# Kernel optimization log

Hardware: AMD Instinct MI355X
Metric: run time of the kernel (lower is better)

Reference implementation:

```python
import jax, jax.numpy as jnp
import numpy as np

EPS = 1e-5
SLOPE = 0.01  # InPlaceABNSync default: leaky_relu(0.01)
SIZES = (1, 2, 3, 6)


def adaptive_avg_pool(x, oh, ow):
    # Matches torch floor/ceil window rule via integral image (single fused op).
    N, C, H, W = x.shape
    S = jnp.pad(x, ((0, 0), (0, 0), (1, 0), (1, 0))).cumsum(2).cumsum(3)
    hs = np.floor(np.arange(oh) * H / oh).astype(np.int32)
    he = np.ceil((np.arange(oh) + 1) * H / oh).astype(np.int32)
    ws = np.floor(np.arange(ow) * W / ow).astype(np.int32)
    we = np.ceil((np.arange(ow) + 1) * W / ow).astype(np.int32)
    sums = (S[:, :, he][:, :, :, we] - S[:, :, hs][:, :, :, we]
            - S[:, :, he][:, :, :, ws] + S[:, :, hs][:, :, :, ws])
    area = ((he - hs)[:, None] * (we - ws)[None, :]).astype(x.dtype)
    return sums / area


def bn_lrelu(x, gamma, beta):
    # BatchNorm (training-mode batch stats, biased var) + leaky_relu, per InPlaceABNSync.
    mean = x.mean((0, 2, 3), keepdims=True)
    var = x.var((0, 2, 3), keepdims=True)
    y = (x - mean) * jax.lax.rsqrt(var + EPS) * gamma[None, :, None, None] + beta[None, :, None, None]
    return jnp.where(y >= 0, y, SLOPE * y)


def upsample_bilinear_ac(x, H, W):
    # align_corners=True bilinear, separable along H then W
    N, C, h, w = x.shape
    yc = jnp.arange(H, dtype=x.dtype) * ((h - 1) / (H - 1) if H > 1 else 0.0)
    xc = jnp.arange(W, dtype=x.dtype) * ((w - 1) / (W - 1) if W > 1 else 0.0)
    y0 = jnp.floor(yc).astype(jnp.int32); y1 = jnp.minimum(y0 + 1, h - 1)
    x0 = jnp.floor(xc).astype(jnp.int32); x1 = jnp.minimum(x0 + 1, w - 1)
    wy = (yc - y0.astype(x.dtype))[None, None, :, None]
    wx = (xc - x0.astype(x.dtype))[None, None, None, :]
    xr = x[:, :, y0, :] * (1 - wy) + x[:, :, y1, :] * wy
    return xr[:, :, :, x0] * (1 - wx) + xr[:, :, :, x1] * wx


def conv1x1(x, w):  # w: [O, I]
    return jnp.einsum('nihw,oi->nohw', x, w)


def conv3x3(x, w):  # w: [O, I, 3, 3]
    return jax.lax.conv_general_dilated(x, w, (1, 1), ((1, 1), (1, 1)),
                                        dimension_numbers=('NCHW', 'OIHW', 'NCHW'))


def setup_inputs() -> dict:
    key = jax.random.key(0)
    ks = jax.random.split(key, 20)
    F_in, F_out = 2048, 512
    inp = {'feats': jax.random.normal(ks[0], (2, F_in, 64, 64), jnp.float32)}
    for s in range(4):
        inp[f'w{s}'] = jax.random.normal(ks[1 + s], (F_out, F_in), jnp.float32) * (F_in ** -0.5)
        inp[f'g{s}'] = jnp.ones((F_out,), jnp.float32)
        inp[f'b{s}'] = jnp.zeros((F_out,), jnp.float32)
    inp['wb'] = jax.random.normal(ks[10], (F_out, F_in + 4 * F_out, 3, 3), jnp.float32) * ((9 * (F_in + 4 * F_out)) ** -0.5)
    inp['gb'] = jnp.ones((F_out,), jnp.float32)
    inp['bb'] = jnp.zeros((F_out,), jnp.float32)
    return inp


def reference(feats, w0, g0, b0, w1, g1, b1, w2, g2, b2, w3, g3, b3, wb, gb, bb):
    H, W = feats.shape[2], feats.shape[3]
    ws = [w0, w1, w2, w3]; gs = [g0, g1, g2, g3]; bs = [b0, b1, b2, b3]
    priors = []
    for s, sz in enumerate(SIZES):
        p = adaptive_avg_pool(feats, sz, sz)
        p = bn_lrelu(conv1x1(p, ws[s]), gs[s], bs[s])
        priors.append(upsample_bilinear_ac(p, H, W))
    priors.append(feats)
    cat = jnp.concatenate(priors, axis=1)
    return bn_lrelu(conv3x3(cat, wb), gb, bb)
```

## Files before the change

### kernel.cpp

```cpp
#include <hip/hip_runtime.h>
#include <stdint.h>


typedef short short8 __attribute__((ext_vector_type(8)));
typedef float f32x4 __attribute__((ext_vector_type(4)));
typedef unsigned short us4 __attribute__((ext_vector_type(4)));

#define PADW   66
#define PLANE  (PADW*PADW)
#define PLANE_ELEMS ((size_t)PLANE*64)

#define POOLED_OFF  0u
#define YS_OFF      819200u
#define STATS_OFF   1024000u
#define CAT_OFF     1048576u
#define CAT_BYTES   71368704u
#define PACKED_OFF  (CAT_OFF + CAT_BYTES)
#define PACKED_BYTES 37748736u
#define CBUF_OFF    (PACKED_OFF + PACKED_BYTES)
#define CBUF_BYTES  16777216u

__device__ __forceinline__ unsigned short f2bf(float x) {
  unsigned int u = __float_as_uint(x);
  unsigned int r = (u + 0x7fffu + ((u >> 16) & 1u)) >> 16;
  return (unsigned short)r;
}

__device__ __forceinline__ void load_lds16(const void* g, uint32_t lds_off) {
  __builtin_amdgcn_global_load_lds(
      (__attribute__((address_space(1))) void*)(uintptr_t)g,
      (__attribute__((address_space(3))) void*)(uintptr_t)lds_off,
      16, 0, 0);
}

__global__ __launch_bounds__(256) void pool_kernel(const float* __restrict__ feats,
                                                   float* __restrict__ pooled) {
  __shared__ float rowtot[64];
  __shared__ float rowseg2[64][2];
  __shared__ float rowseg3[64][3];
  __shared__ float rowseg6[64][6];
  const int t = threadIdx.x;
  const int b = blockIdx.x;
  const float* plane = feats + (size_t)b * 4096;
  const int h = t >> 2, w0 = (t & 3) << 4;
  const int ws3[3] = {0, 21, 42}, we3[3] = {22, 43, 64};
  const int ws6[6] = {0, 10, 21, 32, 42, 53}, we6[6] = {11, 22, 32, 43, 54, 64};
  float p3[3] = {0.f, 0.f, 0.f};
  float p6[6] = {0.f, 0.f, 0.f, 0.f, 0.f, 0.f};
  float tot = 0.f;
  const float4* row = (const float4*)(plane + h * 64 + w0);
#pragma unroll
  for (int i4 = 0; i4 < 4; ++i4) {
    float4 v = row[i4];
    float vals[4] = {v.x, v.y, v.z, v.w};
#pragma unroll
    for (int j = 0; j < 4; ++j) {
      const int w = w0 + i4 * 4 + j;
      const float x = vals[j];
      tot += x;
#pragma unroll
      for (int q = 0; q < 3; ++q) if (w >= ws3[q] && w < we3[q]) p3[q] += x;
#pragma unroll
      for (int q = 0; q < 6; ++q) if (w >= ws6[q] && w < we6[q]) p6[q] += x;
    }
  }
  float pair = tot + __shfl_down(tot, 1, 4);
  float tot4 = pair + __shfl_down(pair, 2, 4);
#pragma unroll
  for (int q = 0; q < 3; ++q) {
    p3[q] += __shfl_down(p3[q], 1, 4);
    p3[q] += __shfl_down(p3[q], 2, 4);
  }
#pragma unroll
  for (int q = 0; q < 6; ++q) {
    p6[q] += __shfl_down(p6[q], 1, 4);
    p6[q] += __shfl_down(p6[q], 2, 4);
  }
  if ((t & 3) == 0) {
    rowtot[h] = tot4;
    rowseg2[h][0] = pair;
#pragma unroll
    for (int q = 0; q < 3; ++q) rowseg3[h][q] = p3[q];
#pragma unroll
    for (int q = 0; q < 6; ++q) rowseg6[h][q] = p6[q];
  }
  if ((t & 3) == 2) rowseg2[h][1] = pair;
  __syncthreads();
  if (t < 50) {
    float s = 0.f;
    float inv;
    if (t == 0) {
      for (int r = 0; r < 64; ++r) s += rowtot[r];
      inv = 1.0f / 4096.0f;
    } else if (t < 5) {
      const int qh = (t - 1) >> 1, qw = (t - 1) & 1;
      for (int r = qh * 32; r < qh * 32 + 32; ++r) s += rowseg2[r][qw];
      inv = 1.0f / 1024.0f;
    } else if (t < 14) {
      const int p = t - 5, qh = p / 3, qw = p % 3;
      for (int r = ws3[qh]; r < we3[qh]; ++r) s += rowseg3[r][qw];
      inv = 1.0f / ((float)(we3[qh] - ws3[qh]) * (float)(we3[qw] - ws3[qw]));
    } else {
      const int p = t - 14, qh = p / 6, qw = p % 6;
      for (int r = ws6[qh]; r < we6[qh]; ++r) s += rowseg6[r][qw];
      inv = 1.0f / ((float)(we6[qh] - ws6[qh]) * (float)(we6[qw] - ws6[qw]));
    }
    const int n = b >> 11, c = b & 2047;
    pooled[((size_t)(n * 50 + t)) * 2048 + c] = s * inv;
  }
}

__global__ __launch_bounds__(256) void conv1x1_kernel(
    const float* __restrict__ pooled, const float* __restrict__ w0,
    const float* __restrict__ w1, const float* __restrict__ w2,
    const float* __restrict__ w3, float* __restrict__ ys) {
  __shared__ float xs[512];
  const int t = threadIdx.x;
  const int col = blockIdx.x >> 2;
  const int kq = blockIdx.x & 3;
  const int n = col / 50, spos = col % 50;
  for (int i = t; i < 512; i += 256)
    xs[i] = pooled[(size_t)col * 2048 + kq * 512 + i];
  __syncthreads();
  int si, pos;
  if (spos < 1)       { si = 0; pos = spos; }
  else if (spos < 5)  { si = 1; pos = spos - 1; }
  else if (spos < 14) { si = 2; pos = spos - 5; }
  else                { si = 3; pos = spos - 14; }
  const float* Wt = (si == 0) ? w0 : (si == 1) ? w1 : (si == 2) ? w2 : w3;
  const int ssarr[4] = {1, 4, 9, 36};
  const int ybase[4] = {0, 1024, 5120, 14336};
  const int ss = ssarr[si];
  for (int o = t; o < 512; o += 256) {
    const float4* wr = (const float4*)(Wt + (size_t)o * 2048 + kq * 512);
    float a = 0.f;
#pragma unroll 4
    for (int c4 = 0; c4 < 128; ++c4) {
      float4 wv = wr[c4];
      a += wv.x * xs[c4 * 4] + wv.y * xs[c4 * 4 + 1] +
           wv.z * xs[c4 * 4 + 2] + wv.w * xs[c4 * 4 + 3];
    }
    atomicAdd(&ys[ybase[si] + (size_t)(n * 512 + o) * ss + pos], a);
  }
}

__global__ __launch_bounds__(512) void bn_small_kernel(
    float* __restrict__ ys, const float* __restrict__ g0, const float* __restrict__ b0,
    const float* __restrict__ g1, const float* __restrict__ b1,
    const float* __restrict__ g2, const float* __restrict__ b2,
    const float* __restrict__ g3, const float* __restrict__ b3) {
  const int si = blockIdx.x;
  const int o = threadIdx.x;
  const int ssarr[4] = {1, 4, 9, 36};
  const int ybase[4] = {0, 1024, 5120, 14336};
  const int ss = ssarr[si];
  const int M = 2 * ss;
  float* base0 = ys + ybase[si] + (size_t)o * ss;
  float* base1 = ys + ybase[si] + (size_t)(512 + o) * ss;
  float sum = 0.f, sq = 0.f;
  for (int p = 0; p < ss; ++p) { float v = base0[p]; sum += v; sq += v * v; }
  for (int p = 0; p < ss; ++p) { float v = base1[p]; sum += v; sq += v * v; }
  const float mean = sum / (float)M;
  float var = sq / (float)M - mean * mean;
  var = fmaxf(var, 0.0f);
  const float rstd = rsqrtf(var + 1e-5f);
  const float* gp = (si == 0) ? g0 : (si == 1) ? g1 : (si == 2) ? g2 : g3;
  const float* bp = (si == 0) ? b0 : (si == 1) ? b1 : (si == 2) ? b2 : b3;
  const float sc = rstd * gp[o];
  const float sh = bp[o] - mean * sc;
  for (int p = 0; p < ss; ++p) {
    float y = base0[p] * sc + sh; base0[p] = (y >= 0.f) ? y : 0.01f * y;
  }
  for (int p = 0; p < ss; ++p) {
    float y = base1[p] * sc + sh; base1[p] = (y >= 0.f) ? y : 0.01f * y;
  }
}

__global__ __launch_bounds__(256) void zero_borders(unsigned short* __restrict__ cat) {
  const int t = threadIdx.x;
  unsigned short* base = cat + (size_t)blockIdx.x * PLANE_ELEMS;
  for (int idx = t; idx < 4160; idx += 256) {
    const int slot = idx >> 4, c4 = idx & 15;
    int q;
    if (slot < 66) q = slot;
    else if (slot < 132) q = 65 * 66 + (slot - 66);
    else { const int k = slot - 132; q = (1 + (k >> 1)) * 66 + (k & 1) * 65; }
    us4 z = {0, 0, 0, 0};
    *(us4*)(base + (size_t)q * 64 + c4 * 4) = z;
  }
}

__global__ __launch_bounds__(256) void fill_priors(const float* __restrict__ ys,
                                                   unsigned short* __restrict__ cat) {
  __shared__ float s0[3072], s1[3072];
  const int t = threadIdx.x;
  const int bx = blockIdx.x;
  const int si = blockIdx.y;
  const int n = bx >> 6, h = bx & 63;
  const int sarr[4] = {1, 2, 3, 6};
  const int ssarr[4] = {1, 4, 9, 36};
  const int ybase[4] = {0, 1024, 5120, 14336};
  const int s = sarr[si], ss = ssarr[si];
  const float yc = (float)(h * (s - 1)) / 63.0f;
  int y0 = (int)yc;
  int y1 = (y0 + 1 < s - 1) ? y0 + 1 : s - 1;
  const float wy = yc - (float)y0;
  const float* base = ys + ybase[si] + (size_t)n * 512 * ss;
  for (int idx = t; idx < 512 * s; idx += 256) {
    int o = idx / s, j = idx - o * s;
    s0[idx] = base[(size_t)o * ss + y0 * s + j];
    s1[idx] = base[(size_t)o * ss + y1 * s + j];
  }
  __syncthreads();
  unsigned short* dstbase = cat + (size_t)(n * 64 + si * 8) * PLANE_ELEMS;
  for (int k = 0; k < 32; ++k) {
    const int g = t + k * 256;
    const int cbp = g >> 10, rem = g & 1023;
    const int w = rem >> 4, c4 = rem & 15;
    const float xc = (float)(w * (s - 1)) / 63.0f;
    int x0 = (int)xc;
    int x1 = (x0 + 1 < s - 1) ? x0 + 1 : s - 1;
    const float wx = xc - (float)x0;
    unsigned short vv[4];
#pragma unroll
    for (int j = 0; j < 4; ++j) {
      const int o = cbp * 64 + c4 * 4 + j;
      const float a = s0[o * s + x0], b2 = s0[o * s + x1];
      const float c = s1[o * s + x0], d = s1[o * s + x1];
      const float top = a + (b2 - a) * wx;
      const float bot = c + (d - c) * wx;
      vv[j] = f2bf(top + (bot - top) * wy);
    }
    us4 ov; ov.x = vv[0]; ov.y = vv[1]; ov.z = vv[2]; ov.w = vv[3];
    const int q = (h + 1) * PADW + (w + 1);
    const int phys = (((c4 >> 1) ^ (q & 7)) << 3) + ((c4 & 1) << 2);
    *(us4*)(dstbase + (size_t)cbp * PLANE_ELEMS + (size_t)q * 64 + phys) = ov;
  }
}

__global__ __launch_bounds__(256) void fill_feats(const float* __restrict__ feats,
                                                  unsigned short* __restrict__ cat) {
  __shared__ float lds[64][65];
  const int t = threadIdx.x;
  const int b = blockIdx.x;
  const int n = b >> 5, fb = b & 31;
  const int h0 = blockIdx.y * 16;
  const float* src = feats + (size_t)(n * 2048 + fb * 64) * 4096;
  unsigned short* dst = cat + (size_t)(n * 64 + 32 + fb) * PLANE_ELEMS;
  for (int h = h0; h < h0 + 16; ++h) {
#pragma unroll
    for (int k = 0; k < 4; ++k) {
      const int idx4 = t + k * 256;
      const int c = idx4 >> 4, w4 = idx4 & 15;
      float4 v = ((const float4*)(src + (size_t)c * 4096 + h * 64))[w4];
      lds[c][w4 * 4 + 0] = v.x; lds[c][w4 * 4 + 1] = v.y;
      lds[c][w4 * 4 + 2] = v.z; lds[c][w4 * 4 + 3] = v.w;
    }
    __syncthreads();
#pragma unroll
    for (int k = 0; k < 4; ++k) {
      const int idx4 = t + k * 256;
      const int w = idx4 >> 4, c4 = idx4 & 15;
      unsigned short vv[4];
#pragma unroll
      for (int j = 0; j < 4; ++j) vv[j] = f2bf(lds[c4 * 4 + j][w]);
      us4 ov; ov.x = vv[0]; ov.y = vv[1]; ov.z = vv[2]; ov.w = vv[3];
      const int q = (h + 1) * PADW + (w + 1);
      const int phys = (((c4 >> 1) ^ (q & 7)) << 3) + ((c4 & 1) << 2);
      *(us4*)(dst + (size_t)q * 64 + phys) = ov;
    }
    __syncthreads();
  }
}

__global__ __launch_bounds__(256) void pack_w(const float* __restrict__ wb,
                                              unsigned short* __restrict__ pk) {
  __shared__ float lds[16][577];
  const int t = threadIdx.x;
  const int cb = blockIdx.x;
  const int ot = blockIdx.y;
  for (int ch8 = 0; ch8 < 8; ++ch8) {
    const int o0 = ot * 128 + ch8 * 16;
    __syncthreads();
#pragma unroll
    for (int k = 0; k < 9; ++k) {
      const int idx4 = t + k * 256;
      const int os = idx4 / 144, c4 = idx4 - os * 144;
      float4 v = ((const float4*)(wb + (size_t)(o0 + os) * 36864 + cb * 576))[c4];
      lds[os][c4 * 4 + 0] = v.x; lds[os][c4 * 4 + 1] = v.y;
      lds[os][c4 * 4 + 2] = v.z; lds[os][c4 * 4 + 3] = v.w;
    }
    __syncthreads();
#pragma unroll
    for (int k = 0; k < 9; ++k) {
      const int g = t + k * 256;
      const int c4 = g & 15;
      const int os = (g >> 4) & 15;
      const int tap = g >> 8;
      unsigned short vv[4];
#pragma unroll
      for (int j = 0; j < 4; ++j) vv[j] = f2bf(lds[os][(c4 * 4 + j) * 9 + tap]);
      us4 ov; ov.x = vv[0]; ov.y = vv[1]; ov.z = vv[2]; ov.w = vv[3];
      const int phys = (((c4 >> 1) ^ (os & 7)) << 3) + ((c4 & 1) << 2);
      const size_t dst = ((size_t)(cb * 9 + tap) * 4 + ot) * 8192 +
                         (size_t)(ch8 * 16 + os) * 64 + phys;
      *(us4*)(pk + dst) = ov;
    }
  }
}

__global__ __launch_bounds__(256, 2) void conv3_kernel(
    const unsigned short* __restrict__ cat, const unsigned short* __restrict__ pk,
    float* __restrict__ C) {
  __shared__ unsigned short As[128 * 64];
  __shared__ unsigned short Bs[128 * 64];
  const int t = threadIdx.x;
  const int lane = t & 63;
  const int wave = t >> 6;
  const int lr = lane & 15;
  const int quad = lane >> 4;
  const int sB = lane & 7;
  const int bx = blockIdx.x;
  const int by = blockIdx.y;
  const int bz = blockIdx.z;
  const int n = bx >> 5;
  const int h0 = (bx & 31) << 1;
  const int wm = wave >> 1, wn = wave & 1;

  f32x4 acc[4][4];
#pragma unroll
  for (int i = 0; i < 4; ++i)
#pragma unroll
    for (int j = 0; j < 4; ++j) acc[i][j] = (f32x4)0.0f;

  const uint32_t as_lds = (uint32_t)(uintptr_t)(&As[0]) + wave * 4096;
  const uint32_t bs_lds = (uint32_t)(uintptr_t)(&Bs[0]) + wave * 4096;
  const uint8_t* catb = (const uint8_t*)cat;
  const uint8_t* pkb = (const uint8_t*)pk;
  const size_t aq_off = ((size_t)(wave >> 1) * PADW * 64 + (size_t)(wave & 1) * 32 * 64) * 2 +
                        (size_t)lane * 16;
  const size_t bq_off = (size_t)wave * 4096 + (size_t)lane * 16;

  for (int cb2 = 0; cb2 < 16; ++cb2) {
    const int cb = bz * 16 + cb2;
    const uint8_t* planeb = catb + (size_t)(n * 64 + cb) * (PLANE_ELEMS * 2);
    for (int tap = 0; tap < 9; ++tap) {
      const int dh = tap / 3 - 1, dw = tap % 3 - 1;
      const int q0 = (h0 + 1 + dh) * PADW + (1 + dw);
      const int sA = (q0 + wm * PADW + lr) & 7;
      __syncthreads();
      const uint8_t* ga = planeb + ((size_t)q0 * 64) * 2 + aq_off;
      const uint8_t* gb = pkb +
          (((size_t)(cb * 9 + tap) * 4 + by) * 8192) * 2 + bq_off;
#pragma unroll
      for (int i = 0; i < 4; ++i) load_lds16(ga + i * 1024, as_lds + i * 1024);
#pragma unroll
      for (int i = 0; i < 4; ++i) load_lds16(gb + i * 1024, bs_lds + i * 1024);
      __syncthreads();
#pragma unroll
      for (int ks = 0; ks < 2; ++ks) {
        const int cA = ((ks * 4 + quad) ^ sA) << 3;
        const int cB = ((ks * 4 + quad) ^ sB) << 3;
        short8 af[4], bf[4];
#pragma unroll
        for (int i = 0; i < 4; ++i)
          af[i] = *(const short8*)(As + (size_t)(wm * 64 + i * 16 + lr) * 64 + cA);
#pragma unroll
        for (int j = 0; j < 4; ++j)
          bf[j] = *(const short8*)(Bs + (size_t)(wn * 64 + j * 16 + lr) * 64 + cB);
#pragma unroll
        for (int i = 0; i < 4; ++i)
#pragma unroll
          for (int j = 0; j < 4; ++j)
            acc[i][j] = __builtin_amdgcn_mfma_f32_16x16x32_bf16(af[i], bf[j],
                                                                acc[i][j], 0, 0, 0);
      }
    }
  }
  const int row4 = quad * 4;
  const int col = lr;
#pragma unroll
  for (int i = 0; i < 4; ++i) {
    const int m0 = wm * 64 + i * 16 + row4;
#pragma unroll
    for (int j = 0; j < 4; ++j) {
      const int o = by * 128 + wn * 64 + j * 16 + col;
#pragma unroll
      for (int r = 0; r < 4; ++r) {
        const size_t p = (size_t)bx * 128 + m0 + r;
        atomicAdd(&C[p * 512 + o], acc[i][j][r]);
      }
    }
  }
}

__global__ __launch_bounds__(256) void bn_stats_kernel(const float* __restrict__ C,
                                                       float* __restrict__ stats) {
  const int t = threadIdx.x;
  const int p0 = blockIdx.x * 32;
  float s0 = 0.f, q0 = 0.f, s1 = 0.f, q1 = 0.f;
  for (int p = p0; p < p0 + 32; ++p) {
    const float a = C[(size_t)p * 512 + t];
    const float b = C[(size_t)p * 512 + t + 256];
    s0 += a; q0 += a * a; s1 += b; q1 += b * b;
  }
  atomicAdd(&stats[t], s0);
  atomicAdd(&stats[t + 256], s1);
  atomicAdd(&stats[512 + t], q0);
  atomicAdd(&stats[512 + t + 256], q1);
}

__global__ __launch_bounds__(256) void bn_apply_kernel(
    const float* __restrict__ C, const float* __restrict__ stats,
    const float* __restrict__ gb, const float* __restrict__ bb,
    float* __restrict__ out) {
  __shared__ float lds[64][65];
  __shared__ float sc_s[64], sh_s[64];
  const int t = threadIdx.x;
  const int p0 = blockIdx.x * 64;
  const int o0 = blockIdx.y * 64;
  if (t < 64) {
    const int o = o0 + t;
    const float mean = stats[o] * (1.0f / 8192.0f);
    float var = stats[512 + o] * (1.0f / 8192.0f) - mean * mean;
    var = fmaxf(var, 0.0f);
    const float rstd = rsqrtf(var + 1e-5f);
    const float sc = rstd * gb[o];
    sc_s[t] = sc;
    sh_s[t] = bb[o] - mean * sc;
  }
#pragma unroll
  for (int k = 0; k < 4; ++k) {
    const int idx4 = t + k * 256;
    const int ps = idx4 >> 4, o4 = idx4 & 15;
    float4 v = ((const float4*)(C + (size_t)(p0 + ps) * 512 + o0))[o4];
    lds[ps][o4 * 4 + 0] = v.x; lds[ps][o4 * 4 + 1] = v.y;
    lds[ps][o4 * 4 + 2] = v.z; lds[ps][o4 * 4 + 3] = v.w;
  }
  __syncthreads();
  const int n = p0 >> 12, h = (p0 >> 6) & 63;
#pragma unroll
  for (int k = 0; k < 4; ++k) {
    const int idx4 = t + k * 256;
    const int os = idx4 >> 4, w4 = idx4 & 15;
    const float sc = sc_s[os], sh = sh_s[os];
    float vv[4];
#pragma unroll
    for (int j = 0; j < 4; ++j) {
      float v = lds[w4 * 4 + j][os] * sc + sh;
      vv[j] = (v >= 0.f) ? v : 0.01f * v;
    }
    float4 r; r.x = vv[0]; r.y = vv[1]; r.z = vv[2]; r.w = vv[3];
    *(float4*)(out + ((size_t)(n * 512 + o0 + os)) * 4096 + h * 64 + w4 * 4) = r;
  }
}

extern "C" void kernel_launch(void* const* d_in, const int* in_sizes, int n_in,
                              void* d_out, int out_size, void* d_ws, size_t ws_size,
                              hipStream_t stream) {
  (void)in_sizes; (void)n_in; (void)out_size; (void)ws_size;
  const float* feats = (const float*)d_in[0];
  const float* w0 = (const float*)d_in[1];
  const float* g0 = (const float*)d_in[2];
  const float* b0 = (const float*)d_in[3];
  const float* w1 = (const float*)d_in[4];
  const float* g1 = (const float*)d_in[5];
  const float* b1 = (const float*)d_in[6];
  const float* w2 = (const float*)d_in[7];
  const float* g2 = (const float*)d_in[8];
  const float* b2 = (const float*)d_in[9];
  const float* w3 = (const float*)d_in[10];
  const float* g3 = (const float*)d_in[11];
  const float* b3 = (const float*)d_in[12];
  const float* wb = (const float*)d_in[13];
  const float* gb = (const float*)d_in[14];
  const float* bb = (const float*)d_in[15];

  uint8_t* ws = (uint8_t*)d_ws;
  float* pooled = (float*)(ws + POOLED_OFF);
  float* ys = (float*)(ws + YS_OFF);
  float* stats = (float*)(ws + STATS_OFF);
  unsigned short* cat = (unsigned short*)(ws + CAT_OFF);
  unsigned short* pk = (unsigned short*)(ws + PACKED_OFF);
  float* C = (float*)(ws + CBUF_OFF);
  float* outp = (float*)d_out;

  hipMemsetAsync(ys, 0, 204800, stream);
  hipMemsetAsync(stats, 0, 4096, stream);
  hipMemsetAsync(C, 0, CBUF_BYTES, stream);

  pool_kernel<<<4096, 256, 0, stream>>>(feats, pooled);
  conv1x1_kernel<<<400, 256, 0, stream>>>(pooled, w0, w1, w2, w3, ys);
  bn_small_kernel<<<4, 512, 0, stream>>>(ys, g0, b0, g1, b1, g2, b2, g3, b3);
  zero_borders<<<128, 256, 0, stream>>>(cat);
  fill_priors<<<dim3(128, 4), 256, 0, stream>>>(ys, cat);
  fill_feats<<<dim3(64, 4), 256, 0, stream>>>(feats, cat);
  pack_w<<<dim3(64, 4), 256, 0, stream>>>(wb, pk);
  conv3_kernel<<<dim3(64, 4, 4), 256, 0, stream>>>(cat, pk, C);
  bn_stats_kernel<<<256, 256, 0, stream>>>(C, stats);
  bn_apply_kernel<<<dim3(128, 8), 256, 0, stream>>>(C, stats, gb, bb, outp);
}
```

Before: 633.6 us.

## Stage four-row input halo once per channel block, read weights directly from global

The conv3x3 kernel now loads a 4-row padded halo (33 KB) of the input plane into LDS once per 64-channel block and reuses it across all nine taps, instead of reloading A and B tiles per tap with two barriers each. Weight fragments are read straight from global memory into registers, using a repacked layout in MFMA fragment order, so B no longer uses LDS. Launch bounds are raised to target three blocks per SM. This cuts LDS traffic and synchronisation, but the weight loads now depend on cache hits and global latency without LDS staging or prefetch.

Result: no change. 633.8 us (+0.0%).

```diff
diff --git a/kernel.cpp b/kernel.cpp
--- a/kernel.cpp
+++ b/kernel.cpp
@@ -301,25 +301,23 @@
 #pragma unroll
       for (int j = 0; j < 4; ++j) vv[j] = f2bf(lds[os][(c4 * 4 + j) * 9 + tap]);
       us4 ov; ov.x = vv[0]; ov.y = vv[1]; ov.z = vv[2]; ov.w = vv[3];
-      const int phys = (((c4 >> 1) ^ (os & 7)) << 3) + ((c4 & 1) << 2);
       const size_t dst = ((size_t)(cb * 9 + tap) * 4 + ot) * 8192 +
-                         (size_t)(ch8 * 16 + os) * 64 + phys;
+                         (size_t)(ch8 * 2 + (c4 >> 3)) * 512 +
+                         (size_t)(((c4 >> 1) & 3) * 16 + os) * 8 + (c4 & 1) * 4;
       *(us4*)(pk + dst) = ov;
     }
   }
 }
 
-__global__ __launch_bounds__(256, 2) void conv3_kernel(
+__global__ __launch_bounds__(256, 3) void conv3_kernel(
     const unsigned short* __restrict__ cat, const unsigned short* __restrict__ pk,
     float* __restrict__ C) {
-  __shared__ unsigned short As[128 * 64];
-  __shared__ unsigned short Bs[128 * 64];
+  __shared__ unsigned short As[264 * 64];
   const int t = threadIdx.x;
   const int lane = t & 63;
   const int wave = t >> 6;
   const int lr = lane & 15;
   const int quad = lane >> 4;
-  const int sB = lane & 7;
   const int bx = blockIdx.x;
   const int by = blockIdx.y;
   const int bz = blockIdx.z;
@@ -333,48 +331,52 @@
 #pragma unroll
     for (int j = 0; j < 4; ++j) acc[i][j] = (f32x4)0.0f;
 
-  const uint32_t as_lds = (uint32_t)(uintptr_t)(&As[0]) + wave * 4096;
-  const uint32_t bs_lds = (uint32_t)(uintptr_t)(&Bs[0]) + wave * 4096;
+  const uint32_t as_base = (uint32_t)(uintptr_t)(&As[0]);
   const uint8_t* catb = (const uint8_t*)cat;
-  const uint8_t* pkb = (const uint8_t*)pk;
-  const size_t aq_off = ((size_t)(wave >> 1) * PADW * 64 + (size_t)(wave & 1) * 32 * 64) * 2 +
-                        (size_t)lane * 16;
-  const size_t bq_off = (size_t)wave * 4096 + (size_t)lane * 16;
+  const unsigned short* pkw = pk + (size_t)by * 8192 + (size_t)(wn * 8) * 512 +
+                              (size_t)lane * 8;
 
   for (int cb2 = 0; cb2 < 16; ++cb2) {
     const int cb = bz * 16 + cb2;
-    const uint8_t* planeb = catb + (size_t)(n * 64 + cb) * (PLANE_ELEMS * 2);
+    const uint8_t* srcA = catb +
+        ((size_t)(n * 64 + cb) * PLANE_ELEMS + (size_t)(h0 * PADW) * 64) * 2;
+    __syncthreads();
+    for (int idx = wave; idx < 33; idx += 4)
+      load_lds16(srcA + (size_t)idx * 1024 + lane * 16,
+                 as_base + (uint32_t)idx * 1024 + lane * 16);
+    __syncthreads();
+#pragma unroll 3
     for (int tap = 0; tap < 9; ++tap) {
       const int dh = tap / 3 - 1, dw = tap % 3 - 1;
-      const int q0 = (h0 + 1 + dh) * PADW + (1 + dw);
-      const int sA = (q0 + wm * PADW + lr) & 7;
-      __syncthreads();
-      const uint8_t* ga = planeb + ((size_t)q0 * 64) * 2 + aq_off;
-      const uint8_t* gb = pkb +
-          (((size_t)(cb * 9 + tap) * 4 + by) * 8192) * 2 + bq_off;
-#pragma unroll
-      for (int i = 0; i < 4; ++i) load_lds16(ga + i * 1024, as_lds + i * 1024);
-#pragma unroll
-      for (int i = 0; i < 4; ++i) load_lds16(gb + i * 1024, bs_lds + i * 1024);
-      __syncthreads();
-#pragma unroll
-      for (int ks = 0; ks < 2; ++ks) {
-        const int cA = ((ks * 4 + quad) ^ sA) << 3;
-        const int cB = ((ks * 4 + quad) ^ sB) << 3;
-        short8 af[4], bf[4];
-#pragma unroll
-        for (int i = 0; i < 4; ++i)
-          af[i] = *(const short8*)(As + (size_t)(wm * 64 + i * 16 + lr) * 64 + cA);
+      const int r = wm + 1 + dh;
+      const unsigned short* pkt = pkw + (size_t)(cb * 9 + tap) * 32768;
+      short8 bf0[4], bf1[4];
+#pragma unroll
+      for (int j = 0; j < 4; ++j) {
+        bf0[j] = *(const short8*)(pkt + (j * 2 + 0) * 512);
+        bf1[j] = *(const short8*)(pkt + (j * 2 + 1) * 512);
+      }
+      short8 af0[4], af1[4];
+#pragma unroll
+      for (int i = 0; i < 4; ++i) {
+        const int s = i * 16 + lr + 1 + dw;
+        const int q = (h0 + r) * PADW + s;
+        const unsigned short* rowp = As + ((r * 66 + s) << 6);
+        af0[i] = *(const short8*)(rowp + ((quad ^ (q & 7)) << 3));
+        af1[i] = *(const short8*)(rowp + (((4 + quad) ^ (q & 7)) << 3));
+      }
+#pragma unroll
+      for (int i = 0; i < 4; ++i)
 #pragma unroll
         for (int j = 0; j < 4; ++j)
-          bf[j] = *(const short8*)(Bs + (size_t)(wn * 64 + j * 16 + lr) * 64 + cB);
-#pragma unroll
-        for (int i = 0; i < 4; ++i)
-#pragma unroll
-          for (int j = 0; j < 4; ++j)
-            acc[i][j] = __builtin_amdgcn_mfma_f32_16x16x32_bf16(af[i], bf[j],
-                                                                acc[i][j], 0, 0, 0);
-      }
+          acc[i][j] = __builtin_amdgcn_mfma_f32_16x16x32_bf16(af0[i], bf0[j],
+                                                              acc[i][j], 0, 0, 0);
+#pragma unroll
+      for (int i = 0; i < 4; ++i)
+#pragma unroll
+        for (int j = 0; j < 4; ++j)
+          acc[i][j] = __builtin_amdgcn_mfma_f32_16x16x32_bf16(af1[i], bf1[j],
+                                                              acc[i][j], 0, 0, 0);
     }
   }
   const int row4 = quad * 4;
```

## Run pyramid 1x1 convs as bf16 MFMA GEMM with packed weights

Applied to the files above, without the earlier changes.

The pool kernel now writes pooled features as bf16 into a padded GEMM A-matrix grouped by pyramid scale. A new wpack1 kernel converts and packs the four 1x1 weight matrices into an MFMA-friendly bf16 layout, and conv1x1_mfma computes the small GEMMs with 16x16x32 bf16 MFMA and writes results directly. This replaces the scalar fp32 dot-product kernel and its atomics, and removes the ys memset. The cost is an extra pack kernel over the 16 MB of weights each call, plus reduced precision in the prior branch.

Result: faster. 600.0 us (-5.3%).

```diff
diff --git a/kernel.cpp b/kernel.cpp
--- a/kernel.cpp
+++ b/kernel.cpp
@@ -10,7 +10,7 @@
 #define PLANE  (PADW*PADW)
 #define PLANE_ELEMS ((size_t)PLANE*64)
 
-#define POOLED_OFF  0u
+#define APOOL_OFF   0u
 #define YS_OFF      819200u
 #define STATS_OFF   1024000u
 #define CAT_OFF     1048576u
@@ -19,6 +19,7 @@
 #define PACKED_BYTES 37748736u
 #define CBUF_OFF    (PACKED_OFF + PACKED_BYTES)
 #define CBUF_BYTES  16777216u
+#define WP_OFF      (CBUF_OFF + CBUF_BYTES)
 
 __device__ __forceinline__ unsigned short f2bf(float x) {
   unsigned int u = __float_as_uint(x);
@@ -34,7 +35,7 @@
 }
 
 __global__ __launch_bounds__(256) void pool_kernel(const float* __restrict__ feats,
-                                                   float* __restrict__ pooled) {
+                                                   unsigned short* __restrict__ apool) {
   __shared__ float rowtot[64];
   __shared__ float rowseg2[64][2];
   __shared__ float rowseg3[64][3];
@@ -89,58 +90,90 @@
   if (t < 50) {
     float s = 0.f;
     float inv;
+    int mrow;
+    const int n = b >> 11, c = b & 2047;
     if (t == 0) {
       for (int r = 0; r < 64; ++r) s += rowtot[r];
       inv = 1.0f / 4096.0f;
+      mrow = n;
     } else if (t < 5) {
       const int qh = (t - 1) >> 1, qw = (t - 1) & 1;
       for (int r = qh * 32; r < qh * 32 + 32; ++r) s += rowseg2[r][qw];
       inv = 1.0f / 1024.0f;
+      mrow = 16 + n * 4 + (t - 1);
     } else if (t < 14) {
       const int p = t - 5, qh = p / 3, qw = p % 3;
       for (int r = ws3[qh]; r < we3[qh]; ++r) s += rowseg3[r][qw];
       inv = 1.0f / ((float)(we3[qh] - ws3[qh]) * (float)(we3[qw] - ws3[qw]));
+      mrow = 32 + n * 9 + p;
     } else {
       const int p = t - 14, qh = p / 6, qw = p % 6;
       for (int r = ws6[qh]; r < we6[qh]; ++r) s += rowseg6[r][qw];
       inv = 1.0f / ((float)(we6[qh] - ws6[qh]) * (float)(we6[qw] - ws6[qw]));
-    }
-    const int n = b >> 11, c = b & 2047;
-    pooled[((size_t)(n * 50 + t)) * 2048 + c] = s * inv;
-  }
-}
-
-__global__ __launch_bounds__(256) void conv1x1_kernel(
-    const float* __restrict__ pooled, const float* __restrict__ w0,
-    const float* __restrict__ w1, const float* __restrict__ w2,
-    const float* __restrict__ w3, float* __restrict__ ys) {
-  __shared__ float xs[512];
-  const int t = threadIdx.x;
-  const int col = blockIdx.x >> 2;
-  const int kq = blockIdx.x & 3;
-  const int n = col / 50, spos = col % 50;
-  for (int i = t; i < 512; i += 256)
-    xs[i] = pooled[(size_t)col * 2048 + kq * 512 + i];
-  __syncthreads();
-  int si, pos;
-  if (spos < 1)       { si = 0; pos = spos; }
-  else if (spos < 5)  { si = 1; pos = spos - 1; }
-  else if (spos < 14) { si = 2; pos = spos - 5; }
-  else                { si = 3; pos = spos - 14; }
+      mrow = 64 + n * 36 + p;
+    }
+    apool[(size_t)mrow * 2048 + c] = f2bf(s * inv);
+  }
+}
+
+__global__ __launch_bounds__(256) void wpack1(
+    const float* __restrict__ w0, const float* __restrict__ w1,
+    const float* __restrict__ w2, const float* __restrict__ w3,
+    unsigned short* __restrict__ wp) {
+  const int t = threadIdx.x;
+  const int si = blockIdx.x >> 5;
+  const int ot = blockIdx.x & 31;
   const float* Wt = (si == 0) ? w0 : (si == 1) ? w1 : (si == 2) ? w2 : w3;
+  const float* base = Wt + (size_t)(ot * 16) * 2048;
+  unsigned short* dst0 = wp + (size_t)(si * 32 + ot) * 64 * 512;
+#pragma unroll
+  for (int i = 0; i < 32; ++i) {
+    const int flat = t + i * 256;
+    const int o = flat >> 9, k4 = flat & 511;
+    float4 v = ((const float4*)(base + (size_t)o * 2048))[k4];
+    unsigned short vv[4] = {f2bf(v.x), f2bf(v.y), f2bf(v.z), f2bf(v.w)};
+    us4 ov; ov.x = vv[0]; ov.y = vv[1]; ov.z = vv[2]; ov.w = vv[3];
+    const int kstep = k4 >> 3, quad = (k4 >> 1) & 3, e0 = (k4 & 1) * 4;
+    *(us4*)(dst0 + (size_t)kstep * 512 + (quad * 16 + o) * 8 + e0) = ov;
+  }
+}
+
+__global__ __launch_bounds__(256) void conv1x1_mfma(
+    const unsigned short* __restrict__ apool, const unsigned short* __restrict__ wp,
+    float* __restrict__ ys) {
+  const int t = threadIdx.x;
+  const int lane = t & 63;
+  const int wv = t >> 6;
+  const int lr = lane & 15;
+  const int quad = lane >> 4;
+  const int mt = blockIdx.x;
+  const int nt = blockIdx.y;
+  const int sitab[9] = {0, 1, 2, 2, 3, 3, 3, 3, 3};
+  const int mbtab[9] = {0, 16, 32, 48, 64, 80, 96, 112, 128};
+  const int si = sitab[mt], mbase = mbtab[mt];
+  const int otile = nt * 4 + wv;
+  const unsigned short* wrec = wp + (size_t)(si * 32 + otile) * 64 * 512 +
+                               (size_t)lane * 8;
+  const unsigned short* arow = apool + (size_t)(mbase + lr) * 2048 + quad * 8;
+  f32x4 acc = (f32x4)0.0f;
+#pragma unroll 4
+  for (int k = 0; k < 64; ++k) {
+    short8 a = *(const short8*)(arow + k * 32);
+    short8 b = *(const short8*)(wrec + (size_t)k * 512);
+    acc = __builtin_amdgcn_mfma_f32_16x16x32_bf16(a, b, acc, 0, 0, 0);
+  }
   const int ssarr[4] = {1, 4, 9, 36};
+  const int mstart[4] = {0, 16, 32, 64};
   const int ybase[4] = {0, 1024, 5120, 14336};
   const int ss = ssarr[si];
-  for (int o = t; o < 512; o += 256) {
-    const float4* wr = (const float4*)(Wt + (size_t)o * 2048 + kq * 512);
-    float a = 0.f;
-#pragma unroll 4
-    for (int c4 = 0; c4 < 128; ++c4) {
-      float4 wv = wr[c4];
-      a += wv.x * xs[c4 * 4] + wv.y * xs[c4 * 4 + 1] +
-           wv.z * xs[c4 * 4 + 2] + wv.w * xs[c4 * 4 + 3];
-    }
-    atomicAdd(&ys[ybase[si] + (size_t)(n * 512 + o) * ss + pos], a);
+  const int o = otile * 16 + lr;
+#pragma unroll
+  for (int r = 0; r < 4; ++r) {
+    const int mr = (mbase - mstart[si]) + quad * 4 + r;
+    if (mr < 2 * ss) {
+      const int n = mr / ss, pos = mr - n * ss;
+      ys[ybase[si] + (size_t)(n * 512 + o) * ss + pos] = acc[r];
+    }
   }
 }
 
@@ -477,20 +510,22 @@
   const float* bb = (const float*)d_in[15];
 
   uint8_t* ws = (uint8_t*)d_ws;
-  float* pooled = (float*)(ws + POOLED_OFF);
+  unsigned short* apool = (unsigned short*)(ws + APOOL_OFF);
   float* ys = (float*)(ws + YS_OFF);
   float* stats = (float*)(ws + STATS_OFF);
   unsigned short* cat = (unsigned short*)(ws + CAT_OFF);
   unsigned short* pk = (unsigned short*)(ws + PACKED_OFF);
   float* C = (float*)(ws + CBUF_OFF);
+  unsigned short* wp = (unsigned short*)(ws + WP_OFF);
   float* outp = (float*)d_out;
 
-  hipMemsetAsync(ys, 0, 204800, stream);
+  hipMemsetAsync(apool, 0, 144 * 2048 * 2, stream);
   hipMemsetAsync(stats, 0, 4096, stream);
   hipMemsetAsync(C, 0, CBUF_BYTES, stream);
 
-  pool_kernel<<<4096, 256, 0, stream>>>(feats, pooled);
-  conv1x1_kernel<<<400, 256, 0, stream>>>(pooled, w0, w1, w2, w3, ys);
+  pool_kernel<<<4096, 256, 0, stream>>>(feats, apool);
+  wpack1<<<128, 256, 0, stream>>>(w0, w1, w2, w3, wp);
+  conv1x1_mfma<<<dim3(9, 8), 256, 0, stream>>>(apool, wp, ys);
   bn_small_kernel<<<4, 512, 0, stream>>>(ys, g0, b0, g1, b1, g2, b2, g3, b3);
   zero_borders<<<128, 256, 0, stream>>>(cat);
   fill_priors<<<dim3(128, 4), 256, 0, stream>>>(ys, cat);
```
